# Kernel tuning notes

Hardware: AMD Instinct MI355X
Metric: run time of the kernel (lower is better)

Reference implementation:

```python
import jax, jax.numpy as jnp
import numpy as np

B, L, D = 32, 256, 1024
H = 8
DQ = D // H            # 128, dim_q == dim_k
DS = 64                # dim_s
DM = 256               # dim_mlp_s
DF = 4096              # dim_feedforward
EPS = 1e-5


def _layernorm(x, g, b):
    mu = jnp.mean(x, axis=-1, keepdims=True)
    var = jnp.mean(jnp.square(x - mu), axis=-1, keepdims=True)
    return (x - mu) * jax.lax.rsqrt(var + EPS) * g + b


def setup_inputs() -> dict:
    key = jax.random.key(0)
    ks = jax.random.split(key, 20)
    s = 0.02
    inp = {
        'src': jax.random.normal(ks[0], (B, L, D), jnp.float32),
        'sf': jax.random.normal(ks[1], (B, DS), jnp.float32),
        'atten_mask': jax.random.randint(ks[2], (B, L, L), 0, 2, jnp.int32),
        # per-head projections, stacked over heads (in,out layout)
        'qw': jax.random.normal(ks[3], (H, D, DQ), jnp.float32) * s,
        'qb': jnp.zeros((H, DQ), jnp.float32),
        'kw': jax.random.normal(ks[4], (H, D, DQ), jnp.float32) * s,
        'kb': jnp.zeros((H, DQ), jnp.float32),
        'vw': jax.random.normal(ks[5], (H, D, DQ), jnp.float32) * s,
        'vb': jnp.zeros((H, DQ), jnp.float32),
        # per-head bias MLP: dim_s -> dim_mlp_s -> L*L
        'b1w': jax.random.normal(ks[6], (H, DS, DM), jnp.float32) * s,
        'b1b': jnp.zeros((H, DM), jnp.float32),
        'b2w': jax.random.normal(ks[7], (H, DM, L * L), jnp.float32) * s,
        'b2b': jnp.zeros((H, L * L), jnp.float32),
        # output projection
        'ow': jax.random.normal(ks[8], (H * DQ, D), jnp.float32) * s,
        'ob': jnp.zeros((D,), jnp.float32),
        # layernorms
        'ln1_g': jnp.ones((D,), jnp.float32), 'ln1_b': jnp.zeros((D,), jnp.float32),
        'ln2_g': jnp.ones((D,), jnp.float32), 'ln2_b': jnp.zeros((D,), jnp.float32),
        # feed-forward
        'w1': jax.random.normal(ks[9], (D, DF), jnp.float32) * s,
        'bf1': jnp.zeros((DF,), jnp.float32),
        'w2': jax.random.normal(ks[10], (DF, D), jnp.float32) * s,
        'bf2': jnp.zeros((D,), jnp.float32),
    }
    return inp


def reference(src, sf, atten_mask, qw, qb, kw, kb, vw, vb, b1w, b1b, b2w, b2b,
              ow, ob, ln1_g, ln1_b, ln2_g, ln2_b, w1, bf1, w2, bf2):
    mask = atten_mask.astype(bool)                      # (B,L,L)
    # per-head projections: (H,B,L,DQ)
    q = jnp.einsum('bld,hdq->hblq', src, qw) + qb[:, None, None, :]
    k = jnp.einsum('bld,hdq->hblq', src, kw) + kb[:, None, None, :]
    v = jnp.einsum('bld,hdq->hblq', src, vw) + vb[:, None, None, :]
    scale = q.shape[-1] ** 0.5
    scores = jnp.einsum('hblq,hbmq->hblm', q, k) / scale
    # masked_fill with constant 1e-9 (NOT -inf), as in the original
    scores = jnp.where(mask[None], jnp.float32(1e-9), scores)
    # per-head learned bias from side features, added AFTER softmax
    hid = jax.nn.relu(jnp.einsum('bs,hsm->hbm', sf, b1w) + b1b[:, None, :])
    bias = (jnp.einsum('hbm,hmn->hbn', hid, b2w) + b2b[:, None, :]).reshape(H, B, L, L)
    soft = jax.nn.softmax(scores, axis=-1) + bias
    out = jnp.einsum('hblm,hbmv->hblv', soft, v)        # (H,B,L,DQ)
    # faithful to original: each head's result is indexed [0] -> batch element 0
    head0 = out[:, 0]                                   # (H,L,DQ)
    hidden = jnp.transpose(head0, (1, 0, 2)).reshape(L, H * DQ)
    attn = hidden @ ow + ob                             # (L,D), broadcasts over batch
    x = _layernorm(src + attn[None], ln1_g, ln1_b)      # (B,L,D)
    ffn = jax.nn.relu(x @ w1 + bf1) @ w2 + bf2
    return _layernorm(x + ffn, ln2_g, ln2_b)
```

## Files before the change

kernel.cpp:

```cpp
#include <hip/hip_runtime.h>

typedef unsigned short u16;
typedef short s16x8 __attribute__((ext_vector_type(8)));
typedef u16 u16x4 __attribute__((ext_vector_type(4)));
typedef float f32x4 __attribute__((ext_vector_type(4)));

#define B_ 32
#define L_ 256
#define D_ 1024
#define H_ 8
#define DQ_ 128
#define DS_ 64
#define DM_ 256
#define DF_ 4096

__device__ __forceinline__ u16 f2bf(float f) {
  unsigned u = __float_as_uint(f);
  unsigned r = (u + 0x7FFFu + ((u >> 16) & 1u)) >> 16;
  return (u16)r;
}
__device__ __forceinline__ float bf2f(u16 x) {
  return __uint_as_float(((unsigned)x) << 16);
}

__device__ __forceinline__ f32x4 mfma16(s16x8 a, s16x8 b, f32x4 c) {
  return __builtin_amdgcn_mfma_f32_16x16x32_bf16(a, b, c, 0, 0, 0);
}

#define GLDS16(g, l)                                                        \
  __builtin_amdgcn_global_load_lds(                                         \
      (__attribute__((address_space(1))) const void*)(g),                   \
      (__attribute__((address_space(3))) void*)(l), 16, 0, 0)

__device__ __forceinline__ void tile_tr(const float* __restrict__ ip,
                                        u16* __restrict__ op, int K, int N,
                                        int bx, int by, float (*t)[33], int tid) {
  const int tx = tid & 31, ty = tid >> 5;
  const long n0 = (long)bx * 32, k0 = (long)by * 32;
#pragma unroll
  for (int i = 0; i < 4; ++i)
    t[ty + i * 8][tx] = ip[(k0 + ty + i * 8) * (long)N + n0 + tx];
  __syncthreads();
#pragma unroll
  for (int i = 0; i < 4; ++i)
    op[(n0 + ty + i * 8) * (long)K + k0 + tx] = f2bf(t[tx][ty + i * 8]);
}

__global__ __launch_bounds__(256) void mega1(
    const float* __restrict__ sf, const float* __restrict__ b1w,
    const float* __restrict__ b1b, const float* __restrict__ b2w,
    const float* __restrict__ b2b, float* __restrict__ biasb,
    const float* __restrict__ src, const float* __restrict__ qw,
    const float* __restrict__ kw, const float* __restrict__ vw,
    const float* __restrict__ qb, const float* __restrict__ kb,
    const float* __restrict__ vb, u16* __restrict__ q0, u16* __restrict__ k0,
    u16* __restrict__ v0T, const float* __restrict__ ow,
    const float* __restrict__ w1, const float* __restrict__ w2,
    u16* __restrict__ owT, u16* __restrict__ w1T, u16* __restrict__ w2T) {
  const int b = blockIdx.x;
  const int tid = threadIdx.x;
  __shared__ float s_sf[DS_];
  __shared__ int wcnt[4];
  __shared__ float sv[DM_];
  __shared__ int si[DM_];
  __shared__ int snnz;
  __shared__ u16 smA[128 * 32];
  __shared__ u16 smB[128 * 40];
  __shared__ float t[32][33];
  if (b < 512) {
    const int h = b >> 6;
    const int n0 = (b & 63) << 10;
    if (tid < DS_) s_sf[tid] = sf[tid];
    __syncthreads();
    float a = b1b[h * DM_ + tid];
    const float* wp = b1w + (long)h * DS_ * DM_ + tid;
#pragma unroll 8
    for (int s = 0; s < DS_; ++s) a += s_sf[s] * wp[s * DM_];
    a = fmaxf(a, 0.f);
    const unsigned long long bal = __ballot(a > 0.f);
    const int lane = tid & 63, wv = tid >> 6;
    const int pc = __popcll(bal);
    if (lane == 0) wcnt[wv] = pc;
    __syncthreads();
    int base = 0;
    for (int i = 0; i < wv; ++i) base += wcnt[i];
    const int pos = base + __popcll(bal & ((1ull << lane) - 1ull));
    if (a > 0.f) { sv[pos] = a; si[pos] = tid; }
    if (tid == 255) snnz = base + pc;
    __syncthreads();
    const int nnz = snnz;
    const float* wb = b2w + (long)h * DM_ * 65536 + n0 + tid * 4;
    float4 acc = {0.f, 0.f, 0.f, 0.f};
    int j = 0;
    for (; j + 4 <= nnz; j += 4) {
      const float4 a0 = *(const float4*)(wb + (long)si[j] * 65536);
      const float4 a1 = *(const float4*)(wb + (long)si[j + 1] * 65536);
      const float4 a2 = *(const float4*)(wb + (long)si[j + 2] * 65536);
      const float4 a3 = *(const float4*)(wb + (long)si[j + 3] * 65536);
      const float v0 = sv[j], v1 = sv[j + 1], v2 = sv[j + 2], v3 = sv[j + 3];
      acc.x += v0 * a0.x + v1 * a1.x + v2 * a2.x + v3 * a3.x;
      acc.y += v0 * a0.y + v1 * a1.y + v2 * a2.y + v3 * a3.y;
      acc.z += v0 * a0.z + v1 * a1.z + v2 * a2.z + v3 * a3.z;
      acc.w += v0 * a0.w + v1 * a1.w + v2 * a2.w + v3 * a3.w;
    }
    for (; j < nnz; ++j) {
      const float4 a0 = *(const float4*)(wb + (long)si[j] * 65536);
      const float v0 = sv[j];
      acc.x += v0 * a0.x; acc.y += v0 * a0.y; acc.z += v0 * a0.z; acc.w += v0 * a0.w;
    }
    const float4 bb = *(const float4*)(b2b + (long)h * 65536 + n0 + tid * 4);
    float4 o = {acc.x + bb.x, acc.y + bb.y, acc.z + bb.z, acc.w + bb.w};
    *(float4*)(biasb + (long)h * 65536 + n0 + tid * 4) = o;
  } else if (b < 560) {
    const int r = b - 512;
    const int z = r >> 1, sel = z >> 3, h = z & 7;
    const long tm = (long)(r & 1) * 128;
    const float* wsrc = (sel == 0 ? qw : (sel == 1 ? kw : vw)) + (long)h * D_ * DQ_;
    const float* bias = (sel == 0 ? qb : (sel == 1 ? kb : vb)) + h * DQ_;
    const int lane = tid & 63;
    const int wv = tid >> 6;
    const int wr = wv >> 1, wc = wv & 1;
    f32x4 acc[4][4];
#pragma unroll
    for (int m = 0; m < 4; ++m)
#pragma unroll
      for (int n = 0; n < 4; ++n) acc[m][n] = (f32x4){0.f, 0.f, 0.f, 0.f};
    for (int k0_ = 0; k0_ < D_; k0_ += 32) {
#pragma unroll
      for (int jj = 0; jj < 4; ++jj) {
        const int f4 = jj * 256 + tid;
        const int row = f4 >> 3, c4 = f4 & 7;
        const float4 v = *(const float4*)(src + (tm + row) * (long)D_ + k0_ + c4 * 4);
        u16x4 o = {f2bf(v.x), f2bf(v.y), f2bf(v.z), f2bf(v.w)};
        *(u16x4*)(&smA[row * 32 + c4 * 4]) = o;
      }
#pragma unroll
      for (int jj = 0; jj < 4; ++jj) {
        const int f4 = jj * 256 + tid;
        const int krow = f4 >> 5, n4 = f4 & 31;
        const float4 v = *(const float4*)(wsrc + (k0_ + krow) * (long)DQ_ + n4 * 4);
        smB[(n4 * 4 + 0) * 40 + krow] = f2bf(v.x);
        smB[(n4 * 4 + 1) * 40 + krow] = f2bf(v.y);
        smB[(n4 * 4 + 2) * 40 + krow] = f2bf(v.z);
        smB[(n4 * 4 + 3) * 40 + krow] = f2bf(v.w);
      }
      __syncthreads();
      s16x8 af[4], bf[4];
      const int ka = (lane >> 4) * 8;
      const int ra = wr * 64 + (lane & 15);
      const int rb = wc * 64 + (lane & 15);
#pragma unroll
      for (int m = 0; m < 4; ++m) af[m] = *(const s16x8*)&smA[(ra + m * 16) * 32 + ka];
#pragma unroll
      for (int n = 0; n < 4; ++n) bf[n] = *(const s16x8*)&smB[(rb + n * 16) * 40 + ka];
#pragma unroll
      for (int m = 0; m < 4; ++m)
#pragma unroll
        for (int n = 0; n < 4; ++n) acc[m][n] = mfma16(af[m], bf[n], acc[m][n]);
      __syncthreads();
    }
    const long crow0 = tm + wr * 64 + ((lane >> 4) * 4);
    const long ccol0 = wc * 64 + (lane & 15);
#pragma unroll
    for (int m = 0; m < 4; ++m)
#pragma unroll
      for (int n = 0; n < 4; ++n)
#pragma unroll
        for (int i = 0; i < 4; ++i) {
          const long row = crow0 + m * 16 + i;
          const long col = ccol0 + n * 16;
          const float v = acc[m][n][i] + bias[col];
          if (sel < 2) {
            u16* o = (sel == 0 ? q0 : k0) + (long)h * L_ * DQ_;
            o[row * DQ_ + col] = f2bf(v);
          } else {
            v0T[(long)h * DQ_ * L_ + col * L_ + row] = f2bf(v);
          }
        }
  } else if (b < 1584) {
    const int rem = b - 560;
    tile_tr(ow, owT, D_, D_, rem & 31, rem >> 5, t, tid);
  } else if (b < 5680) {
    const int rem = b - 1584;
    tile_tr(w1, w1T, D_, DF_, rem & 127, rem >> 7, t, tid);
  } else {
    const int rem = b - 5680;
    tile_tr(w2, w2T, DF_, D_, rem & 31, rem >> 5, t, tid);
  }
}

__global__ __launch_bounds__(64) void attn_kernel(
    const u16* __restrict__ q0, const u16* __restrict__ k0,
    const u16* __restrict__ v0T, const float* __restrict__ biasb,
    const int* __restrict__ mask, u16* __restrict__ hidden) {
  __shared__ char pbuf[8192];
  const int lane = threadIdx.x;
  const int h = blockIdx.y;
  const int r0 = blockIdx.x * 16;
  const int lg = lane >> 4;
  const int ll = lane & 15;
  const u16* q = q0 + (long)h * L_ * DQ_;
  const u16* k = k0 + (long)h * L_ * DQ_;
  const u16* v = v0T + (long)h * DQ_ * L_;

  s16x8 aq[4];
#pragma unroll
  for (int kk = 0; kk < 4; ++kk)
    aq[kk] = *(const s16x8*)(q + (long)(r0 + ll) * DQ_ + kk * 32 + lg * 8);
  float sc[16][4];
  const float scale = 0.08838834764831845f;
#pragma unroll
  for (int t = 0; t < 16; ++t) {
    f32x4 a = {0.f, 0.f, 0.f, 0.f};
#pragma unroll
    for (int kk = 0; kk < 4; ++kk) {
      s16x8 bf = *(const s16x8*)(k + (long)(t * 16 + ll) * DQ_ + kk * 32 + lg * 8);
      a = mfma16(aq[kk], bf, a);
    }
#pragma unroll
    for (int i = 0; i < 4; ++i) {
      const int row = r0 + lg * 4 + i;
      const int col = t * 16 + ll;
      float s = a[i] * scale;
      if (mask[row * L_ + col] != 0) s = 1e-9f;
      sc[t][i] = s;
    }
  }
#pragma unroll
  for (int i = 0; i < 4; ++i) {
    float mx = sc[0][i];
#pragma unroll
    for (int t = 1; t < 16; ++t) mx = fmaxf(mx, sc[t][i]);
#pragma unroll
    for (int d = 1; d < 16; d <<= 1) mx = fmaxf(mx, __shfl_xor(mx, d));
    float sum = 0.f;
#pragma unroll
    for (int t = 0; t < 16; ++t) {
      const float e = __expf(sc[t][i] - mx);
      sc[t][i] = e;
      sum += e;
    }
#pragma unroll
    for (int d = 1; d < 16; d <<= 1) sum += __shfl_xor(sum, d);
    const float inv = 1.f / sum;
    const int row = r0 + lg * 4 + i;
#pragma unroll
    for (int t = 0; t < 16; ++t)
      sc[t][i] = sc[t][i] * inv + biasb[(long)h * 65536 + (long)row * 256 + t * 16 + ll];
  }
#pragma unroll
  for (int t = 0; t < 16; ++t)
#pragma unroll
    for (int i = 0; i < 4; ++i) {
      const int lr = lg * 4 + i;
      const int cb = (t * 16 + ll) * 2;
      *(u16*)(pbuf + lr * 512 + (cb ^ ((lr & 7) << 4))) = f2bf(sc[t][i]);
    }
  s16x8 paf[8];
#pragma unroll
  for (int kk = 0; kk < 8; ++kk)
    paf[kk] = *(const s16x8*)(pbuf + ll * 512 + ((kk * 64 + lg * 16) ^ ((ll & 7) << 4)));
#pragma unroll
  for (int n = 0; n < 8; ++n) {
    f32x4 a = {0.f, 0.f, 0.f, 0.f};
#pragma unroll
    for (int kk = 0; kk < 8; ++kk) {
      s16x8 bf = *(const s16x8*)(v + (long)(n * 16 + ll) * 256 + kk * 32 + lg * 8);
      a = mfma16(paf[kk], bf, a);
    }
#pragma unroll
    for (int i = 0; i < 4; ++i) {
      const int row = r0 + lg * 4 + i;
      const int col = n * 16 + ll;
      hidden[(long)row * 1024 + h * 128 + col] = f2bf(a[i]);
    }
  }
}

__device__ __forceinline__ void g128_core(const u16* __restrict__ A,
                                          const u16* __restrict__ BT, int K,
                                          u16* smA, u16* smB,
                                          f32x4 (&acc)[4][4]) {
  const int tid = threadIdx.x;
  const int lane = tid & 63;
  const int wv = tid >> 6;
  const int wr = wv >> 1, wc = wv & 1;
  const u16* ga = A + (long)(tid >> 2) * K + (tid & 3) * 8;
  const u16* gb = BT + (long)(tid >> 2) * K + (tid & 3) * 8;
  const long rstep = 64L * K;
  u16* la = &smA[tid * 8];
  u16* lb = &smB[tid * 8];
#pragma unroll
  for (int m = 0; m < 4; ++m)
#pragma unroll
    for (int n = 0; n < 4; ++n) acc[m][n] = (f32x4){0.f, 0.f, 0.f, 0.f};
  for (int k0 = 0; k0 < K; k0 += 32) {
    GLDS16(ga + k0, la);
    GLDS16(ga + rstep + k0, la + 64 * 32);
    GLDS16(gb + k0, lb);
    GLDS16(gb + rstep + k0, lb + 64 * 32);
    __syncthreads();
    s16x8 af[4], bf[4];
    const int ka = (lane >> 4) * 8;
    const int ra = wr * 64 + (lane & 15);
    const int rb = wc * 64 + (lane & 15);
#pragma unroll
    for (int m = 0; m < 4; ++m) af[m] = *(const s16x8*)&smA[(ra + m * 16) * 32 + ka];
#pragma unroll
    for (int n = 0; n < 4; ++n) bf[n] = *(const s16x8*)&smB[(rb + n * 16) * 32 + ka];
#pragma unroll
    for (int m = 0; m < 4; ++m)
#pragma unroll
      for (int n = 0; n < 4; ++n) acc[m][n] = mfma16(af[m], bf[n], acc[m][n]);
    __syncthreads();
  }
}

__global__ __launch_bounds__(256) void gemm_bt(
    const u16* __restrict__ A, const u16* __restrict__ BT, float* __restrict__ C,
    const float* __restrict__ bias, int K, int ldc) {
  __shared__ u16 smA[128 * 32];
  __shared__ u16 smB[128 * 32];
  const int tid = threadIdx.x;
  const long tm = (long)blockIdx.x * 128;
  const long tn = (long)blockIdx.y * 128;
  f32x4 acc[4][4];
  g128_core(A + tm * K, BT + tn * K, K, smA, smB, acc);
  const int lane = tid & 63;
  const int wv = tid >> 6;
  const int wr = wv >> 1, wc = wv & 1;
  const long crow0 = tm + wr * 64 + ((lane >> 4) * 4);
  const long ccol0 = tn + wc * 64 + (lane & 15);
#pragma unroll
  for (int m = 0; m < 4; ++m)
#pragma unroll
    for (int n = 0; n < 4; ++n)
#pragma unroll
      for (int i = 0; i < 4; ++i) {
        const long row = crow0 + m * 16 + i;
        const long col = ccol0 + n * 16;
        C[row * (long)ldc + col] = acc[m][n][i] + bias[col];
      }
}

template <int BN, int EPI>
__global__ __launch_bounds__(512, 2) void gemm8p(
    const u16* __restrict__ A, const u16* __restrict__ BT, void* __restrict__ Cv,
    const float* __restrict__ bias, const void* __restrict__ R, int M, int N,
    int K, int ldc) {
  extern __shared__ char lds[];
  constexpr int NR = BN / 64;
  constexpr int NHB = BN / 128;
  constexpr int BUF = 32768 + BN * 128;
  constexpr int WST = (NHB == 2) ? 4 : 2;
  const int tid = threadIdx.x;
  const int lane = tid & 63;
  const int w = tid >> 6;
  const int wr = w >> 2, wc = w & 3;

  const int total = gridDim.x;
  int bid = blockIdx.x;
  int s = ((total & 7) == 0) ? ((bid & 7) * (total >> 3) + (bid >> 3)) : bid;
  const int gn = N / BN;
  const long tm = (long)(s / gn) * 256;
  const long tn = (long)(s % gn) * BN;
  const int NT = K >> 6;

  auto stageA = [&](int half, int t) {
    char* hb = lds + (long)(t & 1) * BUF + half * 16384;
    const u16* g = A + (tm + half * 128) * (long)K + (long)t * 64;
#pragma unroll
    for (int j = 0; j < 2; ++j) {
      const int idx = j * 512 + tid;
      const int r = idx >> 3;
      const int c16 = (idx & 7) ^ (r & 7);
      GLDS16(g + (long)r * K + c16 * 8, hb + idx * 16);
    }
  };
  auto stageB = [&](int half, int t) {
    char* hb = lds + (long)(t & 1) * BUF + 32768 + half * 16384;
    const u16* g = BT + (tn + half * 128) * (long)K + (long)t * 64;
#pragma unroll
    for (int j = 0; j < 2; ++j) {
      const int idx = j * 512 + tid;
      const int r = idx >> 3;
      const int c16 = (idx & 7) ^ (r & 7);
      GLDS16(g + (long)r * K + c16 * 8, hb + idx * 16);
    }
  };

  stageA(0, 0);
  stageA(1, 0);
  stageB(0, 0);
  if (NHB == 2) stageB(1, 0);
  stageB(0, 1);
  if (NHB == 2) stageB(1, 1);
  asm volatile("s_waitcnt vmcnt(%0)" ::"n"(WST) : "memory");
  __builtin_amdgcn_s_barrier();

  f32x4 acc[8][NR];
#pragma unroll
  for (int m = 0; m < 8; ++m)
#pragma unroll
    for (int n = 0; n < NR; ++n) acc[m][n] = (f32x4){0.f, 0.f, 0.f, 0.f};

  const int lk = (lane >> 4) * 16;
  const int lr = lane & 15;

  for (int t = 0; t < NT; ++t) {
    const char* bp = lds + (long)(t & 1) * BUF;
    s16x8 bfr[NR][2];
#pragma unroll
    for (int p = 0; p < 4; ++p) {
      if (p == 0) {
#pragma unroll
        for (int ni = 0; ni < NR; ++ni) {
          const int brow = wc * (BN / 4) + ni * 16 + lr;
#pragma unroll
          for (int ks = 0; ks < 2; ++ks) {
            const int kb = (ks * 64 + lk) ^ ((brow & 7) << 4);
            bfr[ni][ks] = *(const s16x8*)(bp + 32768 + brow * 128 + kb);
          }
        }
      }
      s16x8 afr[2][2];
#pragma unroll
      for (int rI = 0; rI < 2; ++rI) {
        const int arow = wr * 128 + (2 * p + rI) * 16 + lr;
#pragma unroll
        for (int ks = 0; ks < 2; ++ks) {
          const int kb = (ks * 64 + lk) ^ ((arow & 7) << 4);
          afr[rI][ks] = *(const s16x8*)(bp + arow * 128 + kb);
        }
      }
      if (p == 0) { if (t + 1 < NT) stageA(0, t + 1); }
      else if (p == 1) { if (t + 1 < NT) stageA(1, t + 1); }
      else if (p == 2) { if (t + 2 < NT) stageB(0, t + 2); }
      else { if (NHB == 2 && t + 2 < NT) stageB(1, t + 2); }
      __builtin_amdgcn_s_barrier();
      __builtin_amdgcn_s_setprio(1);
#pragma unroll
      for (int rI = 0; rI < 2; ++rI)
#pragma unroll
        for (int ni = 0; ni < NR; ++ni)
#pragma unroll
          for (int ks = 0; ks < 2; ++ks)
            acc[2 * p + rI][ni] = mfma16(afr[rI][ks], bfr[ni][ks], acc[2 * p + rI][ni]);
      __builtin_amdgcn_s_setprio(0);
      if (p == 3) {
        if (t + 2 < NT) {
          asm volatile("s_waitcnt vmcnt(%0)" ::"n"(WST) : "memory");
        } else if (t + 1 < NT) {
          asm volatile("s_waitcnt vmcnt(0)" ::: "memory");
        }
      }
      __builtin_amdgcn_s_barrier();
    }
  }

  const long crow0 = tm + wr * 128 + ((lane >> 4) * 4);
  const long ccol0 = tn + wc * (BN / 4) + lr;
#pragma unroll
  for (int m = 0; m < 8; ++m) {
#pragma unroll
    for (int n = 0; n < NR; ++n) {
#pragma unroll
      for (int i = 0; i < 4; ++i) {
        const long row = crow0 + m * 16 + i;
        const long col = ccol0 + n * 16;
        const float v = acc[m][n][i] + bias[col];
        if constexpr (EPI == 1) {
          ((u16*)Cv)[row * (long)ldc + col] = f2bf(fmaxf(v, 0.f));
        } else {
          const float r = bf2f(((const u16*)R)[row * (long)ldc + col]);
          ((u16*)Cv)[row * (long)ldc + col] = f2bf(v + r);
        }
      }
    }
  }
}

template <int MODE>
__global__ __launch_bounds__(256) void ln_kernel(
    const void* __restrict__ in0v, const float* __restrict__ add1,
    const float* __restrict__ g, const float* __restrict__ bb,
    void* __restrict__ outv) {
  const int tid = threadIdx.x;
  const long row = blockIdx.x;
  float4 v;
  if constexpr (MODE == 0) {
    v = ((const float4*)((const float*)in0v + row * D_))[tid];
    const float4 u = ((const float4*)(add1 + (row & (L_ - 1)) * D_))[tid];
    v.x += u.x; v.y += u.y; v.z += u.z; v.w += u.w;
  } else {
    const uint2 pk = *(const uint2*)((const u16*)in0v + row * D_ + tid * 4);
    v.x = __uint_as_float((pk.x & 0xFFFFu) << 16);
    v.y = __uint_as_float(pk.x & 0xFFFF0000u);
    v.z = __uint_as_float((pk.y & 0xFFFFu) << 16);
    v.w = __uint_as_float(pk.y & 0xFFFF0000u);
  }
  float s = v.x + v.y + v.z + v.w;
  float q = v.x * v.x + v.y * v.y + v.z * v.z + v.w * v.w;
#pragma unroll
  for (int d = 1; d < 64; d <<= 1) { s += __shfl_xor(s, d); q += __shfl_xor(q, d); }
  __shared__ float ss[4], sq[4];
  const int wv = tid >> 6;
  if ((tid & 63) == 0) { ss[wv] = s; sq[wv] = q; }
  __syncthreads();
  s = ss[0] + ss[1] + ss[2] + ss[3];
  q = sq[0] + sq[1] + sq[2] + sq[3];
  const float mu = s * (1.f / D_);
  const float var = q * (1.f / D_) - mu * mu;
  const float rs = rsqrtf(var + 1e-5f);
  const float4 gv = ((const float4*)g)[tid];
  const float4 bv = ((const float4*)bb)[tid];
  float4 o;
  o.x = (v.x - mu) * rs * gv.x + bv.x;
  o.y = (v.y - mu) * rs * gv.y + bv.y;
  o.z = (v.z - mu) * rs * gv.z + bv.z;
  o.w = (v.w - mu) * rs * gv.w + bv.w;
  if constexpr (MODE == 0) {
    uint2 pk;
    pk.x = (unsigned)f2bf(o.x) | ((unsigned)f2bf(o.y) << 16);
    pk.y = (unsigned)f2bf(o.z) | ((unsigned)f2bf(o.w) << 16);
    *(uint2*)((u16*)outv + row * D_ + tid * 4) = pk;
  } else {
    ((float4*)((float*)outv + row * D_))[tid] = o;
  }
}

extern "C" void kernel_launch(void* const* d_in, const int* in_sizes, int n_in,
                              void* d_out, int out_size, void* d_ws, size_t ws_size,
                              hipStream_t stream) {
  (void)in_sizes; (void)n_in; (void)out_size; (void)ws_size;
  const float* src = (const float*)d_in[0];
  const float* sf = (const float*)d_in[1];
  const int* mask = (const int*)d_in[2];
  const float* qw = (const float*)d_in[3];
  const float* qb = (const float*)d_in[4];
  const float* kw = (const float*)d_in[5];
  const float* kb = (const float*)d_in[6];
  const float* vw = (const float*)d_in[7];
  const float* vb = (const float*)d_in[8];
  const float* b1w = (const float*)d_in[9];
  const float* b1b = (const float*)d_in[10];
  const float* b2w = (const float*)d_in[11];
  const float* b2b = (const float*)d_in[12];
  const float* ow = (const float*)d_in[13];
  const float* ob = (const float*)d_in[14];
  const float* ln1g = (const float*)d_in[15];
  const float* ln1b = (const float*)d_in[16];
  const float* ln2g = (const float*)d_in[17];
  const float* ln2b = (const float*)d_in[18];
  const float* w1 = (const float*)d_in[19];
  const float* bf1 = (const float*)d_in[20];
  const float* w2 = (const float*)d_in[21];
  const float* bf2 = (const float*)d_in[22];
  float* out = (float*)d_out;

  char* ws = (char*)d_ws;
  size_t off = 0;
  auto alloc = [&](size_t bytes) {
    void* p = ws + off;
    off += (bytes + 255) & ~(size_t)255;
    return p;
  };
  u16* owT = (u16*)alloc((size_t)D_ * D_ * 2);
  u16* w1T = (u16*)alloc((size_t)DF_ * D_ * 2);
  u16* w2T = (u16*)alloc((size_t)D_ * DF_ * 2);
  u16* q0 = (u16*)alloc((size_t)H_ * L_ * DQ_ * 2);
  u16* k0 = (u16*)alloc((size_t)H_ * L_ * DQ_ * 2);
  u16* v0T = (u16*)alloc((size_t)H_ * DQ_ * L_ * 2);
  float* biasb = (float*)alloc((size_t)H_ * L_ * L_ * 4);
  u16* hidden = (u16*)alloc((size_t)L_ * D_ * 2);
  float* attnvec = (float*)alloc((size_t)L_ * D_ * 4);
  u16* xb = (u16*)alloc((size_t)B_ * L_ * D_ * 2);
  u16* ffnh = (u16*)alloc((size_t)B_ * L_ * DF_ * 2);
  u16* yb = (u16*)alloc((size_t)B_ * L_ * D_ * 2);

  hipFuncSetAttribute((const void*)gemm8p<256, 1>,
                      hipFuncAttributeMaxDynamicSharedMemorySize, 131072);
  hipFuncSetAttribute((const void*)gemm8p<128, 2>,
                      hipFuncAttributeMaxDynamicSharedMemorySize, 98304);

  const dim3 b256(256);
  mega1<<<dim3(9776), b256, 0, stream>>>(sf, b1w, b1b, b2w, b2b, biasb, src, qw,
                                         kw, vw, qb, kb, vb, q0, k0, v0T, ow, w1,
                                         w2, owT, w1T, w2T);
  attn_kernel<<<dim3(16, H_), dim3(64), 0, stream>>>(q0, k0, v0T, biasb, mask,
                                                     hidden);
  gemm_bt<<<dim3(2, 8), b256, 0, stream>>>(hidden, owT, attnvec, ob, D_, D_);
  ln_kernel<0><<<dim3(B_ * L_), b256, 0, stream>>>(src, attnvec, ln1g, ln1b, xb);
  gemm8p<256, 1><<<dim3(512), dim3(512), 131072, stream>>>(
      xb, w1T, ffnh, bf1, nullptr, B_ * L_, DF_, D_, DF_);
  gemm8p<128, 2><<<dim3(256), dim3(512), 98304, stream>>>(
      ffnh, w2T, yb, bf2, xb, B_ * L_, D_, DF_, D_);
  ln_kernel<1><<<dim3(B_ * L_), b256, 0, stream>>>(yb, nullptr, ln2g, ln2b, out);
}
```

Baseline: 358.5 us.

## Split prep into transpose kernel and use async LDS loads for QKV GEMM

Splits the fused first kernel in two. The new first kernel transposes and converts to bf16 all weights, including the Q/K/V projections, plus batch-0 of src. The second kernel runs the bias MLP and a QKV GEMM that now reads pre-converted bf16 tiles through global_load_lds instead of converting fp32 in registers and scattering into LDS. The QKV GEMM was likely the long tail of the old kernel, while transposes of 48 GEMM blocks were cheap. The cost is an extra launch, extra workspace traffic for the transposed QKV weights, and an unpadded LDS layout for B that may cause bank conflicts.

```diff
diff --git a/kernel.cpp b/kernel.cpp
--- a/kernel.cpp
+++ b/kernel.cpp
@@ -46,17 +46,49 @@
     op[(n0 + ty + i * 8) * (long)K + k0 + tx] = f2bf(t[tx][ty + i * 8]);
 }
 
-__global__ __launch_bounds__(256) void mega1(
+__global__ __launch_bounds__(256) void prep(
+    const float* __restrict__ qw, const float* __restrict__ kw,
+    const float* __restrict__ vw, const float* __restrict__ src,
+    const float* __restrict__ ow, const float* __restrict__ w1,
+    const float* __restrict__ w2, u16* __restrict__ qwT, u16* __restrict__ kwT,
+    u16* __restrict__ vwT, u16* __restrict__ src0b, u16* __restrict__ owT,
+    u16* __restrict__ w1T, u16* __restrict__ w2T) {
+  const int b = blockIdx.x;
+  const int tid = threadIdx.x;
+  __shared__ float t[32][33];
+  if (b < 3072) {
+    const int z = b >> 7, rem = b & 127;
+    const int sel = z >> 3, h = z & 7;
+    const float* ip = (sel == 0 ? qw : (sel == 1 ? kw : vw)) + (long)h * D_ * DQ_;
+    u16* op = (sel == 0 ? qwT : (sel == 1 ? kwT : vwT)) + (long)h * DQ_ * D_;
+    tile_tr(ip, op, D_, DQ_, rem & 3, rem >> 2, t, tid);
+  } else if (b < 3328) {
+    const int rem = b - 3072;
+    const int i = (rem * 256 + tid) * 4;
+    float4 v = *(const float4*)(src + i);
+    u16x4 o = {f2bf(v.x), f2bf(v.y), f2bf(v.z), f2bf(v.w)};
+    *(u16x4*)(src0b + i) = o;
+  } else if (b < 4352) {
+    const int rem = b - 3328;
+    tile_tr(ow, owT, D_, D_, rem & 31, rem >> 5, t, tid);
+  } else if (b < 8448) {
+    const int rem = b - 4352;
+    tile_tr(w1, w1T, D_, DF_, rem & 127, rem >> 7, t, tid);
+  } else {
+    const int rem = b - 8448;
+    tile_tr(w2, w2T, DF_, D_, rem & 31, rem >> 5, t, tid);
+  }
+}
+
+__global__ __launch_bounds__(256) void phase2(
     const float* __restrict__ sf, const float* __restrict__ b1w,
     const float* __restrict__ b1b, const float* __restrict__ b2w,
     const float* __restrict__ b2b, float* __restrict__ biasb,
-    const float* __restrict__ src, const float* __restrict__ qw,
-    const float* __restrict__ kw, const float* __restrict__ vw,
+    const u16* __restrict__ src0b, const u16* __restrict__ qwT,
+    const u16* __restrict__ kwT, const u16* __restrict__ vwT,
     const float* __restrict__ qb, const float* __restrict__ kb,
     const float* __restrict__ vb, u16* __restrict__ q0, u16* __restrict__ k0,
-    u16* __restrict__ v0T, const float* __restrict__ ow,
-    const float* __restrict__ w1, const float* __restrict__ w2,
-    u16* __restrict__ owT, u16* __restrict__ w1T, u16* __restrict__ w2T) {
+    u16* __restrict__ v0T) {
   const int b = blockIdx.x;
   const int tid = threadIdx.x;
   __shared__ float s_sf[DS_];
@@ -65,8 +97,7 @@
   __shared__ int si[DM_];
   __shared__ int snnz;
   __shared__ u16 smA[128 * 32];
-  __shared__ u16 smB[128 * 40];
-  __shared__ float t[32][33];
+  __shared__ u16 smB[128 * 32];
   if (b < 512) {
     const int h = b >> 6;
     const int n0 = (b & 63) << 10;
@@ -111,39 +142,31 @@
     const float4 bb = *(const float4*)(b2b + (long)h * 65536 + n0 + tid * 4);
     float4 o = {acc.x + bb.x, acc.y + bb.y, acc.z + bb.z, acc.w + bb.w};
     *(float4*)(biasb + (long)h * 65536 + n0 + tid * 4) = o;
-  } else if (b < 560) {
+  } else {
     const int r = b - 512;
     const int z = r >> 1, sel = z >> 3, h = z & 7;
     const long tm = (long)(r & 1) * 128;
-    const float* wsrc = (sel == 0 ? qw : (sel == 1 ? kw : vw)) + (long)h * D_ * DQ_;
+    const int K = D_;
+    const u16* BT = (sel == 0 ? qwT : (sel == 1 ? kwT : vwT)) + (long)h * DQ_ * D_;
     const float* bias = (sel == 0 ? qb : (sel == 1 ? kb : vb)) + h * DQ_;
     const int lane = tid & 63;
     const int wv = tid >> 6;
     const int wr = wv >> 1, wc = wv & 1;
+    const u16* ga = src0b + (tm + (tid >> 2)) * (long)K + (tid & 3) * 8;
+    const u16* gb = BT + (long)(tid >> 2) * K + (tid & 3) * 8;
+    const long rstep = 64L * K;
+    u16* la = &smA[tid * 8];
+    u16* lb = &smB[tid * 8];
     f32x4 acc[4][4];
 #pragma unroll
     for (int m = 0; m < 4; ++m)
 #pragma unroll
       for (int n = 0; n < 4; ++n) acc[m][n] = (f32x4){0.f, 0.f, 0.f, 0.f};
-    for (int k0_ = 0; k0_ < D_; k0_ += 32) {
-#pragma unroll
-      for (int jj = 0; jj < 4; ++jj) {
-        const int f4 = jj * 256 + tid;
-        const int row = f4 >> 3, c4 = f4 & 7;
-        const float4 v = *(const float4*)(src + (tm + row) * (long)D_ + k0_ + c4 * 4);
-        u16x4 o = {f2bf(v.x), f2bf(v.y), f2bf(v.z), f2bf(v.w)};
-        *(u16x4*)(&smA[row * 32 + c4 * 4]) = o;
-      }
-#pragma unroll
-      for (int jj = 0; jj < 4; ++jj) {
-        const int f4 = jj * 256 + tid;
-        const int krow = f4 >> 5, n4 = f4 & 31;
-        const float4 v = *(const float4*)(wsrc + (k0_ + krow) * (long)DQ_ + n4 * 4);
-        smB[(n4 * 4 + 0) * 40 + krow] = f2bf(v.x);
-        smB[(n4 * 4 + 1) * 40 + krow] = f2bf(v.y);
-        smB[(n4 * 4 + 2) * 40 + krow] = f2bf(v.z);
-        smB[(n4 * 4 + 3) * 40 + krow] = f2bf(v.w);
-      }
+    for (int k0_ = 0; k0_ < K; k0_ += 32) {
+      GLDS16(ga + k0_, la);
+      GLDS16(ga + rstep + k0_, la + 64 * 32);
+      GLDS16(gb + k0_, lb);
+      GLDS16(gb + rstep + k0_, lb + 64 * 32);
       __syncthreads();
       s16x8 af[4], bf[4];
       const int ka = (lane >> 4) * 8;
@@ -152,7 +175,7 @@
 #pragma unroll
       for (int m = 0; m < 4; ++m) af[m] = *(const s16x8*)&smA[(ra + m * 16) * 32 + ka];
 #pragma unroll
-      for (int n = 0; n < 4; ++n) bf[n] = *(const s16x8*)&smB[(rb + n * 16) * 40 + ka];
+      for (int n = 0; n < 4; ++n) bf[n] = *(const s16x8*)&smB[(rb + n * 16) * 32 + ka];
 #pragma unroll
       for (int m = 0; m < 4; ++m)
 #pragma unroll
@@ -177,15 +200,6 @@
             v0T[(long)h * DQ_ * L_ + col * L_ + row] = f2bf(v);
           }
         }
-  } else if (b < 1584) {
-    const int rem = b - 560;
-    tile_tr(ow, owT, D_, D_, rem & 31, rem >> 5, t, tid);
-  } else if (b < 5680) {
-    const int rem = b - 1584;
-    tile_tr(w1, w1T, D_, DF_, rem & 127, rem >> 7, t, tid);
-  } else {
-    const int rem = b - 5680;
-    tile_tr(w2, w2T, DF_, D_, rem & 31, rem >> 5, t, tid);
   }
 }
 
@@ -565,9 +579,13 @@
     off += (bytes + 255) & ~(size_t)255;
     return p;
   };
+  u16* qwT = (u16*)alloc((size_t)H_ * DQ_ * D_ * 2);
+  u16* kwT = (u16*)alloc((size_t)H_ * DQ_ * D_ * 2);
+  u16* vwT = (u16*)alloc((size_t)H_ * DQ_ * D_ * 2);
   u16* owT = (u16*)alloc((size_t)D_ * D_ * 2);
   u16* w1T = (u16*)alloc((size_t)DF_ * D_ * 2);
   u16* w2T = (u16*)alloc((size_t)D_ * DF_ * 2);
+  u16* src0b = (u16*)alloc((size_t)L_ * D_ * 2);
   u16* q0 = (u16*)alloc((size_t)H_ * L_ * DQ_ * 2);
   u16* k0 = (u16*)alloc((size_t)H_ * L_ * DQ_ * 2);
   u16* v0T = (u16*)alloc((size_t)H_ * DQ_ * L_ * 2);
@@ -584,9 +602,10 @@
                       hipFuncAttributeMaxDynamicSharedMemorySize, 98304);
 
   const dim3 b256(256);
-  mega1<<<dim3(9776), b256, 0, stream>>>(sf, b1w, b1b, b2w, b2b, biasb, src, qw,
-                                         kw, vw, qb, kb, vb, q0, k0, v0T, ow, w1,
-                                         w2, owT, w1T, w2T);
+  prep<<<dim3(12544), b256, 0, stream>>>(qw, kw, vw, src, ow, w1, w2, qwT, kwT,
+                                         vwT, src0b, owT, w1T, w2T);
+  phase2<<<dim3(560), b256, 0, stream>>>(sf, b1w, b1b, b2w, b2b, biasb, src0b,
+                                         qwT, kwT, vwT, qb, kb, vb, q0, k0, v0T);
   attn_kernel<<<dim3(16, H_), dim3(64), 0, stream>>>(q0, k0, v0T, biasb, mask,
                                                      hidden);
   gemm_bt<<<dim3(2, 8), b256, 0, stream>>>(hidden, owT, attnvec, ob, D_, D_);
```

Measured after the change: 330.3 us. -7.9%, faster.
